# Kernel tuning notes

Measured on AMD Instinct MI355X. Metric: run time of the kernel, lower is better.

Reference implementation:

```python
import jax, jax.numpy as jnp
import numpy as np

NUM_BLOCKS = 2
NUM_LAYERS = 10
DILATIONS = tuple(2 ** d for _ in range(NUM_BLOCKS) for d in range(NUM_LAYERS))  # 20 layers
B, CIN, C, T = 8, 1, 128, 16384
L = len(DILATIONS)


def setup_inputs() -> dict:
    key = jax.random.key(0)
    ks = jax.random.split(key, 12)
    s = 0.1  # weight scale ~ kaiming-ish for C=128
    return {
        "x": jax.random.normal(ks[0], (B, CIN, T), jnp.float32),
        "W_in": jax.random.normal(ks[1], (C, CIN, 1), jnp.float32) * 0.5,
        "b_in": jnp.zeros((C,), jnp.float32),
        "W_dil": jax.random.normal(ks[2], (L, C, C, 2), jnp.float32) * s,
        "b_dil": jnp.zeros((L, C), jnp.float32),
        "W_tanh": jax.random.normal(ks[3], (L, C, C, 1), jnp.float32) * s,
        "b_tanh": jnp.zeros((L, C), jnp.float32),
        "W_sig": jax.random.normal(ks[4], (L, C, C, 1), jnp.float32) * s,
        "b_sig": jnp.zeros((L, C), jnp.float32),
        "W_skip": jax.random.normal(ks[5], (L, C, C, 1), jnp.float32) * s,
        "b_skip": jnp.zeros((L, C), jnp.float32),
    }


def _conv1x1(w, b, x):
    # w: [O, I, 1], x: [B, I, T] -> [B, O, T]
    return jnp.einsum('oi,bit->bot', w[:, :, 0], x) + b[None, :, None]


def _dilated_causal_conv(x, w, b, dilation):
    # causal pad left by (kernel_size-1)*dilation = dilation, then dilated conv k=2
    xp = jnp.pad(x, ((0, 0), (0, 0), (dilation, 0)))
    y = jax.lax.conv_general_dilated(
        xp, w, window_strides=(1,), padding=[(0, 0)],
        rhs_dilation=(dilation,), dimension_numbers=('NCW', 'OIW', 'NCW'))
    return y + b[None, :, None]


def reference(x, W_in, b_in, W_dil, b_dil, W_tanh, b_tanh, W_sig, b_sig, W_skip, b_skip):
    h = _conv1x1(W_in, b_in, x)  # [B, C, T]
    skip_agg = jnp.zeros_like(h[:, :1, :]) * 0.0  # placeholder; replaced on first add
    skip_agg = 0.0
    for l, dil in enumerate(DILATIONS):
        xd = _dilated_causal_conv(h, W_dil[l], b_dil[l], dil)
        f = jnp.tanh(_conv1x1(W_tanh[l], b_tanh[l], xd))
        g = jax.nn.sigmoid(_conv1x1(W_sig[l], b_sig[l], xd))
        xh = g * f
        skip_agg = skip_agg + _conv1x1(W_skip[l], b_skip[l], xh)
        h = xh + xd  # faithful: residual adds dilated-conv output, not layer input
    return skip_agg
```

## Files before the change

kernel.cpp:

```cpp
#include <hip/hip_runtime.h>

#define B_ 8
#define C_ 128
#define T_ 16384
#define L_ 20
#define TN 128
#define NTL (T_ / TN)
#define XROW 136
#define WROW 40

typedef short bf16x8 __attribute__((ext_vector_type(8)));
typedef float f32x16 __attribute__((ext_vector_type(16)));

__device__ __forceinline__ ushort bf16_rn(float v) {
    union { float f; unsigned u; } a; a.f = v;
    unsigned r = (a.u + 0x7FFFu + ((a.u >> 16) & 1u)) >> 16;
    return (ushort)r;
}
__device__ __forceinline__ float bf16_to_f(ushort h) {
    union { unsigned u; float f; } b; b.u = ((unsigned)h) << 16;
    return b.f;
}
__device__ __forceinline__ void split2(float v, ushort& hh, ushort& ll) {
    ushort h = bf16_rn(v);
    hh = h;
    ll = bf16_rn(v - bf16_to_f(h));
}

__global__ __launch_bounds__(256) void prep_kernel(
    const float* __restrict__ Wd, const float* __restrict__ Wt,
    const float* __restrict__ Ws, const float* __restrict__ Wk,
    ushort* __restrict__ WdH, ushort* __restrict__ WdL,
    ushort* __restrict__ WtH, ushort* __restrict__ WtL,
    ushort* __restrict__ WsH, ushort* __restrict__ WsL,
    ushort* __restrict__ WkH, ushort* __restrict__ WkL)
{
    int idx = blockIdx.x * 256 + threadIdx.x;
    const int ND = L_ * C_ * 256;
    const int N1 = L_ * C_ * C_;
    float v; ushort* oH; ushort* oL; int o;
    if (idx < ND) {
        int k = idx & 255, m = (idx >> 8) & 127, l = idx >> 15;
        v = Wd[(((size_t)(l * C_ + m)) * C_ + (k & 127)) * 2 + (k >> 7)];
        oH = WdH; oL = WdL; o = idx;
    } else {
        int i2 = idx - ND;
        if (i2 < N1)            { v = Wt[i2]; oH = WtH; oL = WtL; o = i2; }
        else if (i2 < 2 * N1)   { o = i2 - N1;     v = Ws[o]; oH = WsH; oL = WsL; }
        else if (i2 < 3 * N1)   { o = i2 - 2 * N1; v = Wk[o]; oH = WkH; oL = WkL; }
        else return;
    }
    ushort h, l; split2(v, h, l);
    oH[o] = h; oL[o] = l;
}

__global__ __launch_bounds__(256) void in_conv_kernel(
    const float* __restrict__ x, const float* __restrict__ Win,
    const float* __restrict__ bin, float* __restrict__ h)
{
    int idx = blockIdx.x * 256 + threadIdx.x;
    int t4 = idx & (T_ / 4 - 1);
    int bc = idx >> 12;
    int c = bc & 127;
    float w = Win[c], bias = bin[c];
    const float4 xv = *(const float4*)(x + ((size_t)(bc >> 7)) * T_ + (size_t)t4 * 4);
    float4 o;
    o.x = w * xv.x + bias; o.y = w * xv.y + bias;
    o.z = w * xv.z + bias; o.w = w * xv.w + bias;
    *(float4*)(h + (size_t)bc * T_ + (size_t)t4 * 4) = o;
}

__device__ __forceinline__ void stageX(
    const float* __restrict__ hb, int tbase,
    ushort* __restrict__ XH, ushort* __restrict__ XL)
{
    __syncthreads();
    const int tid = threadIdx.x;
    const int tl = tid & 127, cg = tid >> 7;
    const int tg = tbase + tl;
    const bool ok = (tg >= 0);
    #pragma unroll
    for (int j = 0; j < 8; ++j) {
        int c0 = cg * 32 + j * 4;
        float v0 = ok ? hb[(c0 + 0) * T_ + tg] : 0.f;
        float v1 = ok ? hb[(c0 + 1) * T_ + tg] : 0.f;
        float v2 = ok ? hb[(c0 + 2) * T_ + tg] : 0.f;
        float v3 = ok ? hb[(c0 + 3) * T_ + tg] : 0.f;
        ushort4 h4, l4;
        split2(v0, h4.x, l4.x); split2(v1, h4.y, l4.y);
        split2(v2, h4.z, l4.z); split2(v3, h4.w, l4.w);
        *(ushort4*)&XH[tl * XROW + c0] = h4;
        *(ushort4*)&XL[tl * XROW + c0] = l4;
    }
    __syncthreads();
}

__device__ __forceinline__ void gemm_one(
    const ushort* __restrict__ gH, const ushort* __restrict__ gL,
    int rowlen, int kw0,
    ushort* __restrict__ sH, ushort* __restrict__ sL,
    const ushort* __restrict__ XH, const ushort* __restrict__ XL,
    int m_wave, int n_wave, int ln31, int kg,
    f32x16 (&acc)[2])
{
    const int tid = threadIdx.x;
    const int sm = tid >> 2, sk = (tid & 3) * 8;
    const int gbase = sm * rowlen + kw0 + sk;
    uint4 pH = *(const uint4*)(gH + gbase);
    uint4 pL = *(const uint4*)(gL + gbase);
    #pragma unroll
    for (int c = 0; c < 4; ++c) {
        __syncthreads();
        *(uint4*)&sH[sm * WROW + sk] = pH;
        *(uint4*)&sL[sm * WROW + sk] = pL;
        int kn = (c < 3) ? (c + 1) * 32 : 3 * 32;
        pH = *(const uint4*)(gH + gbase + kn);
        pL = *(const uint4*)(gL + gbase + kn);
        __syncthreads();
        #pragma unroll
        for (int ks = 0; ks < 32; ks += 16) {
            bf16x8 bh = *(const bf16x8*)&XH[(n_wave + ln31) * XROW + c * 32 + ks + kg];
            bf16x8 bl = *(const bf16x8*)&XL[(n_wave + ln31) * XROW + c * 32 + ks + kg];
            #pragma unroll
            for (int mi = 0; mi < 2; ++mi) {
                bf16x8 ah = *(const bf16x8*)&sH[(m_wave + mi * 32 + ln31) * WROW + ks + kg];
                bf16x8 al = *(const bf16x8*)&sL[(m_wave + mi * 32 + ln31) * WROW + ks + kg];
                acc[mi] = __builtin_amdgcn_mfma_f32_32x32x16_bf16(ah, bh, acc[mi], 0, 0, 0);
                acc[mi] = __builtin_amdgcn_mfma_f32_32x32x16_bf16(ah, bl, acc[mi], 0, 0, 0);
                acc[mi] = __builtin_amdgcn_mfma_f32_32x32x16_bf16(al, bh, acc[mi], 0, 0, 0);
            }
        }
    }
}

__device__ __forceinline__ void gemm_two(
    const ushort* __restrict__ gH0, const ushort* __restrict__ gL0,
    const ushort* __restrict__ gH1, const ushort* __restrict__ gL1,
    ushort* __restrict__ sH0, ushort* __restrict__ sL0,
    ushort* __restrict__ sH1, ushort* __restrict__ sL1,
    const ushort* __restrict__ XH, const ushort* __restrict__ XL,
    int m_wave, int n_wave, int ln31, int kg,
    f32x16 (&a0)[2], f32x16 (&a1)[2])
{
    const int tid = threadIdx.x;
    const int sm = tid >> 2, sk = (tid & 3) * 8;
    const int gbase = sm * 128 + sk;
    uint4 pH0 = *(const uint4*)(gH0 + gbase);
    uint4 pL0 = *(const uint4*)(gL0 + gbase);
    uint4 pH1 = *(const uint4*)(gH1 + gbase);
    uint4 pL1 = *(const uint4*)(gL1 + gbase);
    #pragma unroll
    for (int c = 0; c < 4; ++c) {
        __syncthreads();
        *(uint4*)&sH0[sm * WROW + sk] = pH0;
        *(uint4*)&sL0[sm * WROW + sk] = pL0;
        *(uint4*)&sH1[sm * WROW + sk] = pH1;
        *(uint4*)&sL1[sm * WROW + sk] = pL1;
        int kn = (c < 3) ? (c + 1) * 32 : 3 * 32;
        pH0 = *(const uint4*)(gH0 + gbase + kn);
        pL0 = *(const uint4*)(gL0 + gbase + kn);
        pH1 = *(const uint4*)(gH1 + gbase + kn);
        pL1 = *(const uint4*)(gL1 + gbase + kn);
        __syncthreads();
        #pragma unroll
        for (int ks = 0; ks < 32; ks += 16) {
            bf16x8 bh = *(const bf16x8*)&XH[(n_wave + ln31) * XROW + c * 32 + ks + kg];
            bf16x8 bl = *(const bf16x8*)&XL[(n_wave + ln31) * XROW + c * 32 + ks + kg];
            #pragma unroll
            for (int mi = 0; mi < 2; ++mi) {
                int ai = (m_wave + mi * 32 + ln31) * WROW + ks + kg;
                bf16x8 ah0 = *(const bf16x8*)&sH0[ai];
                bf16x8 al0 = *(const bf16x8*)&sL0[ai];
                bf16x8 ah1 = *(const bf16x8*)&sH1[ai];
                bf16x8 al1 = *(const bf16x8*)&sL1[ai];
                a0[mi] = __builtin_amdgcn_mfma_f32_32x32x16_bf16(ah0, bh, a0[mi], 0, 0, 0);
                a0[mi] = __builtin_amdgcn_mfma_f32_32x32x16_bf16(ah0, bl, a0[mi], 0, 0, 0);
                a0[mi] = __builtin_amdgcn_mfma_f32_32x32x16_bf16(al0, bh, a0[mi], 0, 0, 0);
                a1[mi] = __builtin_amdgcn_mfma_f32_32x32x16_bf16(ah1, bh, a1[mi], 0, 0, 0);
                a1[mi] = __builtin_amdgcn_mfma_f32_32x32x16_bf16(ah1, bl, a1[mi], 0, 0, 0);
                a1[mi] = __builtin_amdgcn_mfma_f32_32x32x16_bf16(al1, bh, a1[mi], 0, 0, 0);
            }
        }
    }
}

__global__ __launch_bounds__(512, 2) void layer_kernel(
    const float* __restrict__ h_in, float* __restrict__ h_out,
    float* __restrict__ skip,
    const ushort* __restrict__ WdH, const ushort* __restrict__ WdL,
    const ushort* __restrict__ WtH, const ushort* __restrict__ WtL,
    const ushort* __restrict__ WsH, const ushort* __restrict__ WsL,
    const ushort* __restrict__ WkH, const ushort* __restrict__ WkL,
    const float* __restrict__ bd, const float* __restrict__ bt,
    const float* __restrict__ bs, const float* __restrict__ bk,
    int dil, int addskip)
{
    __shared__ ushort XbH[TN * XROW], XbL[TN * XROW];
    __shared__ ushort WaH[C_ * WROW], WaL[C_ * WROW];
    __shared__ ushort WbH[C_ * WROW], WbL[C_ * WROW];
    __shared__ float bias_lds[512];

    const int tid = threadIdx.x;
    const int b  = blockIdx.x / NTL;
    const int t0 = (blockIdx.x % NTL) * TN;
    const int lane = tid & 63;
    const int wave = tid >> 6;
    const int m_wave = (wave & 1) * 64;
    const int n_wave = (wave >> 1) * 32;
    const int ln31 = lane & 31, kg = (lane >> 5) * 8, hi5 = lane >> 5;
    const float* hb = h_in + (size_t)b * C_ * T_;

    {
        int sec = tid >> 7;
        const float* bp = sec == 0 ? bd : (sec == 1 ? bt : (sec == 2 ? bs : bk));
        bias_lds[tid] = bp[tid & 127];
    }

    f32x16 xdacc[2];
    #pragma unroll
    for (int mi = 0; mi < 2; ++mi)
        #pragma unroll
        for (int r = 0; r < 16; ++r) xdacc[mi][r] = 0.f;

    stageX(hb, t0 - dil, XbH, XbL);
    gemm_one(WdH, WdL, 256, 0,   WaH, WaL, XbH, XbL, m_wave, n_wave, ln31, kg, xdacc);
    stageX(hb, t0,       XbH, XbL);
    gemm_one(WdH, WdL, 256, 128, WaH, WaL, XbH, XbL, m_wave, n_wave, ln31, kg, xdacc);

    __syncthreads();
    const int nn = n_wave + ln31;
    #pragma unroll
    for (int mi = 0; mi < 2; ++mi) {
        #pragma unroll
        for (int g = 0; g < 4; ++g) {
            int mloc = m_wave + mi * 32 + g * 8 + 4 * hi5;
            const float* bb = &bias_lds[mloc];
            ushort4 h4, l4;
            float v0 = xdacc[mi][g * 4 + 0] + bb[0]; xdacc[mi][g * 4 + 0] = v0;
            float v1 = xdacc[mi][g * 4 + 1] + bb[1]; xdacc[mi][g * 4 + 1] = v1;
            float v2 = xdacc[mi][g * 4 + 2] + bb[2]; xdacc[mi][g * 4 + 2] = v2;
            float v3 = xdacc[mi][g * 4 + 3] + bb[3]; xdacc[mi][g * 4 + 3] = v3;
            split2(v0, h4.x, l4.x); split2(v1, h4.y, l4.y);
            split2(v2, h4.z, l4.z); split2(v3, h4.w, l4.w);
            *(ushort4*)&XbH[nn * XROW + mloc] = h4;
            *(ushort4*)&XbL[nn * XROW + mloc] = l4;
        }
    }

    f32x16 at[2], as_[2];
    #pragma unroll
    for (int mi = 0; mi < 2; ++mi)
        #pragma unroll
        for (int r = 0; r < 16; ++r) { at[mi][r] = 0.f; as_[mi][r] = 0.f; }
    gemm_two(WtH, WtL, WsH, WsL, WaH, WaL, WbH, WbL,
             XbH, XbL, m_wave, n_wave, ln31, kg, at, as_);

    __syncthreads();
    float* hob = h_out + (size_t)b * C_ * T_;
    f32x16 xhv[2];
    #pragma unroll
    for (int mi = 0; mi < 2; ++mi) {
        #pragma unroll
        for (int g = 0; g < 4; ++g) {
            int mloc = m_wave + mi * 32 + g * 8 + 4 * hi5;
            const float* btp = &bias_lds[128 + mloc];
            const float* bsp = &bias_lds[256 + mloc];
            ushort4 h4, l4;
            #pragma unroll
            for (int j = 0; j < 4; ++j) {
                float a = at[mi][g * 4 + j] + btp[j];
                float s = as_[mi][g * 4 + j] + bsp[j];
                float f  = 2.f / (1.f + __expf(-2.f * a)) - 1.f;
                float gg = 1.f / (1.f + __expf(-s));
                float xh = f * gg;
                xhv[mi][g * 4 + j] = xh;
                ushort hh, ll; split2(xh, hh, ll);
                ((ushort*)&h4)[j] = hh; ((ushort*)&l4)[j] = ll;
                hob[(size_t)(mloc + j) * T_ + t0 + nn] = xh + xdacc[mi][g * 4 + j];
            }
            *(ushort4*)&XbH[nn * XROW + mloc] = h4;
            *(ushort4*)&XbL[nn * XROW + mloc] = l4;
        }
    }

    f32x16 ak[2];
    #pragma unroll
    for (int mi = 0; mi < 2; ++mi)
        #pragma unroll
        for (int r = 0; r < 16; ++r) ak[mi][r] = 0.f;
    gemm_one(WkH, WkL, 128, 0, WaH, WaL, XbH, XbL, m_wave, n_wave, ln31, kg, ak);

    float* skb = skip + (size_t)b * C_ * T_;
    #pragma unroll
    for (int mi = 0; mi < 2; ++mi) {
        #pragma unroll
        for (int g = 0; g < 4; ++g) {
            int mloc = m_wave + mi * 32 + g * 8 + 4 * hi5;
            const float* bkp = &bias_lds[384 + mloc];
            #pragma unroll
            for (int j = 0; j < 4; ++j) {
                float v = ak[mi][g * 4 + j] + bkp[j];
                size_t adr = (size_t)(mloc + j) * T_ + t0 + nn;
                if (addskip) v += skb[adr];
                skb[adr] = v;
            }
        }
    }
}

extern "C" void kernel_launch(void* const* d_in, const int* in_sizes, int n_in,
                              void* d_out, int out_size, void* d_ws, size_t ws_size,
                              hipStream_t stream)
{
    const float* x   = (const float*)d_in[0];
    const float* Win = (const float*)d_in[1];
    const float* bin = (const float*)d_in[2];
    const float* Wd  = (const float*)d_in[3];
    const float* bd  = (const float*)d_in[4];
    const float* Wt  = (const float*)d_in[5];
    const float* bt  = (const float*)d_in[6];
    const float* Ws  = (const float*)d_in[7];
    const float* bs  = (const float*)d_in[8];
    const float* Wk  = (const float*)d_in[9];
    const float* bk  = (const float*)d_in[10];
    float* out = (float*)d_out;

    float* ws = (float*)d_ws;
    const size_t HN = (size_t)B_ * C_ * T_;
    float* hA = ws;
    float* hB = ws + HN;
    ushort* wb = (ushort*)(ws + 2 * HN);
    const size_t ND = (size_t)L_ * C_ * 256;
    const size_t N1 = (size_t)L_ * C_ * C_;
    ushort* WdH = wb;            ushort* WdL = WdH + ND;
    ushort* WtH = WdL + ND;      ushort* WtL = WtH + N1;
    ushort* WsH = WtL + N1;      ushort* WsL = WsH + N1;
    ushort* WkH = WsL + N1;      ushort* WkL = WkH + N1;

    const int prep_total = (int)(ND + 3 * N1);
    prep_kernel<<<(prep_total + 255) / 256, 256, 0, stream>>>(
        Wd, Wt, Ws, Wk, WdH, WdL, WtH, WtL, WsH, WsL, WkH, WkL);
    in_conv_kernel<<<(B_ * C_ * (T_ / 4)) / 256, 256, 0, stream>>>(x, Win, bin, hA);

    float* hin = hA;
    float* hout = hB;
    for (int l = 0; l < L_; ++l) {
        int dil = 1 << (l % 10);
        layer_kernel<<<B_ * NTL, 512, 0, stream>>>(
            hin, hout, out,
            WdH + (size_t)l * C_ * 256, WdL + (size_t)l * C_ * 256,
            WtH + (size_t)l * C_ * C_,  WtL + (size_t)l * C_ * C_,
            WsH + (size_t)l * C_ * C_,  WsL + (size_t)l * C_ * C_,
            WkH + (size_t)l * C_ * C_,  WkL + (size_t)l * C_ * C_,
            bd + l * C_, bt + l * C_, bs + l * C_, bk + l * C_,
            dil, l > 0 ? 1 : 0);
        float* tmp = hin; hin = hout; hout = tmp;
    }
}
```

Before: 2.778 ms.

## Shrink LDS with XOR-swizzled layouts and 16-wide K chunks for higher occupancy

Weights are pre-tiled on the host-side prep kernel into 16-wide K chunks with an XOR swizzle, and the activation tile drops its row padding in favour of an XOR swizzle, so LDS per block shrinks enough to raise launch bounds from 2 to 4 blocks per CU. The fused tanh/sigmoid GEMM is split into two sequential single-weight GEMMs, removing the second weight buffer, and the dilated-conv output is recovered from LDS instead of being held in registers. The cost is twice as many K-chunk barriers and smaller per-chunk weight loads, plus register pressure under the tighter launch bound.

```diff
diff --git a/kernel.cpp b/kernel.cpp
--- a/kernel.cpp
+++ b/kernel.cpp
@@ -6,11 +6,12 @@
 #define L_ 20
 #define TN 128
 #define NTL (T_ / TN)
-#define XROW 136
-#define WROW 40
+#define XROW 128
+#define WROW 16
 
 typedef short bf16x8 __attribute__((ext_vector_type(8)));
 typedef float f32x16 __attribute__((ext_vector_type(16)));
+typedef unsigned short u16x8 __attribute__((ext_vector_type(8)));
 
 __device__ __forceinline__ ushort bf16_rn(float v) {
     union { float f; unsigned u; } a; a.f = v;
@@ -42,16 +43,21 @@
     if (idx < ND) {
         int k = idx & 255, m = (idx >> 8) & 127, l = idx >> 15;
         v = Wd[(((size_t)(l * C_ + m)) * C_ + (k & 127)) * 2 + (k >> 7)];
-        oH = WdH; oL = WdL; o = idx;
+        o = l * (C_ * 256) + (k >> 4) * 2048 + m * WROW + ((k & 15) ^ ((m & 1) << 3));
+        oH = WdH; oL = WdL;
     } else {
         int i2 = idx - ND;
-        if (i2 < N1)            { v = Wt[i2]; oH = WtH; oL = WtL; o = i2; }
-        else if (i2 < 2 * N1)   { o = i2 - N1;     v = Ws[o]; oH = WsH; oL = WsL; }
-        else if (i2 < 3 * N1)   { o = i2 - 2 * N1; v = Wk[o]; oH = WkH; oL = WkL; }
+        const float* src;
+        if (i2 < N1)           { src = Wt; oH = WtH; oL = WtL; }
+        else if (i2 < 2 * N1)  { i2 -= N1;     src = Ws; oH = WsH; oL = WsL; }
+        else if (i2 < 3 * N1)  { i2 -= 2 * N1; src = Wk; oH = WkH; oL = WkL; }
         else return;
-    }
-    ushort h, l; split2(v, h, l);
-    oH[o] = h; oL[o] = l;
+        int k = i2 & 127, m = (i2 >> 7) & 127, l = i2 >> 14;
+        v = src[i2];
+        o = l * (C_ * C_) + (k >> 4) * 2048 + m * WROW + ((k & 15) ^ ((m & 1) << 3));
+    }
+    ushort h, l2; split2(v, h, l2);
+    oH[o] = h; oL[o] = l2;
 }
 
 __global__ __launch_bounds__(256) void in_conv_kernel(
@@ -79,112 +85,62 @@
     const int tl = tid & 127, cg = tid >> 7;
     const int tg = tbase + tl;
     const bool ok = (tg >= 0);
-    #pragma unroll
-    for (int j = 0; j < 8; ++j) {
-        int c0 = cg * 32 + j * 4;
-        float v0 = ok ? hb[(c0 + 0) * T_ + tg] : 0.f;
-        float v1 = ok ? hb[(c0 + 1) * T_ + tg] : 0.f;
-        float v2 = ok ? hb[(c0 + 2) * T_ + tg] : 0.f;
-        float v3 = ok ? hb[(c0 + 3) * T_ + tg] : 0.f;
-        ushort4 h4, l4;
-        split2(v0, h4.x, l4.x); split2(v1, h4.y, l4.y);
-        split2(v2, h4.z, l4.z); split2(v3, h4.w, l4.w);
-        *(ushort4*)&XH[tl * XROW + c0] = h4;
-        *(ushort4*)&XL[tl * XROW + c0] = l4;
+    const int sw = (tl & 7) << 3;
+    #pragma unroll
+    for (int j = 0; j < 4; ++j) {
+        int c0 = cg * 32 + j * 8;
+        u16x8 h8, l8;
+        #pragma unroll
+        for (int i = 0; i < 8; ++i) {
+            float v = ok ? hb[(size_t)(c0 + i) * T_ + tg] : 0.f;
+            ushort hh, ll; split2(v, hh, ll);
+            h8[i] = hh; l8[i] = ll;
+        }
+        *(u16x8*)&XH[tl * XROW + (c0 ^ sw)] = h8;
+        *(u16x8*)&XL[tl * XROW + (c0 ^ sw)] = l8;
     }
     __syncthreads();
 }
 
-__device__ __forceinline__ void gemm_one(
-    const ushort* __restrict__ gH, const ushort* __restrict__ gL,
-    int rowlen, int kw0,
+__device__ __forceinline__ void gemm16(
+    const ushort* __restrict__ gH, const ushort* __restrict__ gL, int kc0,
     ushort* __restrict__ sH, ushort* __restrict__ sL,
     const ushort* __restrict__ XH, const ushort* __restrict__ XL,
-    int m_wave, int n_wave, int ln31, int kg,
+    int m_wave, int nn, int ln31, int kg,
     f32x16 (&acc)[2])
 {
     const int tid = threadIdx.x;
-    const int sm = tid >> 2, sk = (tid & 3) * 8;
-    const int gbase = sm * rowlen + kw0 + sk;
-    uint4 pH = *(const uint4*)(gH + gbase);
-    uint4 pL = *(const uint4*)(gL + gbase);
-    #pragma unroll
-    for (int c = 0; c < 4; ++c) {
+    const int e = tid * 4;
+    const ushort* gph = gH + kc0 * 2048 + e;
+    const ushort* gpl = gL + kc0 * 2048 + e;
+    uint2 pH = *(const uint2*)gph;
+    uint2 pL = *(const uint2*)gpl;
+    const int nsw = (nn & 7) << 3;
+    const int a0 = (m_wave + ln31) * WROW + (kg ^ ((ln31 & 1) << 3));
+    #pragma unroll
+    for (int c = 0; c < 8; ++c) {
         __syncthreads();
-        *(uint4*)&sH[sm * WROW + sk] = pH;
-        *(uint4*)&sL[sm * WROW + sk] = pL;
-        int kn = (c < 3) ? (c + 1) * 32 : 3 * 32;
-        pH = *(const uint4*)(gH + gbase + kn);
-        pL = *(const uint4*)(gL + gbase + kn);
+        *(uint2*)&sH[e] = pH;
+        *(uint2*)&sL[e] = pL;
+        int nx = ((c < 7) ? (c + 1) : 7) * 2048;
+        pH = *(const uint2*)(gph + nx);
+        pL = *(const uint2*)(gpl + nx);
         __syncthreads();
-        #pragma unroll
-        for (int ks = 0; ks < 32; ks += 16) {
-            bf16x8 bh = *(const bf16x8*)&XH[(n_wave + ln31) * XROW + c * 32 + ks + kg];
-            bf16x8 bl = *(const bf16x8*)&XL[(n_wave + ln31) * XROW + c * 32 + ks + kg];
-            #pragma unroll
-            for (int mi = 0; mi < 2; ++mi) {
-                bf16x8 ah = *(const bf16x8*)&sH[(m_wave + mi * 32 + ln31) * WROW + ks + kg];
-                bf16x8 al = *(const bf16x8*)&sL[(m_wave + mi * 32 + ln31) * WROW + ks + kg];
-                acc[mi] = __builtin_amdgcn_mfma_f32_32x32x16_bf16(ah, bh, acc[mi], 0, 0, 0);
-                acc[mi] = __builtin_amdgcn_mfma_f32_32x32x16_bf16(ah, bl, acc[mi], 0, 0, 0);
-                acc[mi] = __builtin_amdgcn_mfma_f32_32x32x16_bf16(al, bh, acc[mi], 0, 0, 0);
-            }
-        }
-    }
-}
-
-__device__ __forceinline__ void gemm_two(
-    const ushort* __restrict__ gH0, const ushort* __restrict__ gL0,
-    const ushort* __restrict__ gH1, const ushort* __restrict__ gL1,
-    ushort* __restrict__ sH0, ushort* __restrict__ sL0,
-    ushort* __restrict__ sH1, ushort* __restrict__ sL1,
-    const ushort* __restrict__ XH, const ushort* __restrict__ XL,
-    int m_wave, int n_wave, int ln31, int kg,
-    f32x16 (&a0)[2], f32x16 (&a1)[2])
-{
-    const int tid = threadIdx.x;
-    const int sm = tid >> 2, sk = (tid & 3) * 8;
-    const int gbase = sm * 128 + sk;
-    uint4 pH0 = *(const uint4*)(gH0 + gbase);
-    uint4 pL0 = *(const uint4*)(gL0 + gbase);
-    uint4 pH1 = *(const uint4*)(gH1 + gbase);
-    uint4 pL1 = *(const uint4*)(gL1 + gbase);
-    #pragma unroll
-    for (int c = 0; c < 4; ++c) {
-        __syncthreads();
-        *(uint4*)&sH0[sm * WROW + sk] = pH0;
-        *(uint4*)&sL0[sm * WROW + sk] = pL0;
-        *(uint4*)&sH1[sm * WROW + sk] = pH1;
-        *(uint4*)&sL1[sm * WROW + sk] = pL1;
-        int kn = (c < 3) ? (c + 1) * 32 : 3 * 32;
-        pH0 = *(const uint4*)(gH0 + gbase + kn);
-        pL0 = *(const uint4*)(gL0 + gbase + kn);
-        pH1 = *(const uint4*)(gH1 + gbase + kn);
-        pL1 = *(const uint4*)(gL1 + gbase + kn);
-        __syncthreads();
-        #pragma unroll
-        for (int ks = 0; ks < 32; ks += 16) {
-            bf16x8 bh = *(const bf16x8*)&XH[(n_wave + ln31) * XROW + c * 32 + ks + kg];
-            bf16x8 bl = *(const bf16x8*)&XL[(n_wave + ln31) * XROW + c * 32 + ks + kg];
-            #pragma unroll
-            for (int mi = 0; mi < 2; ++mi) {
-                int ai = (m_wave + mi * 32 + ln31) * WROW + ks + kg;
-                bf16x8 ah0 = *(const bf16x8*)&sH0[ai];
-                bf16x8 al0 = *(const bf16x8*)&sL0[ai];
-                bf16x8 ah1 = *(const bf16x8*)&sH1[ai];
-                bf16x8 al1 = *(const bf16x8*)&sL1[ai];
-                a0[mi] = __builtin_amdgcn_mfma_f32_32x32x16_bf16(ah0, bh, a0[mi], 0, 0, 0);
-                a0[mi] = __builtin_amdgcn_mfma_f32_32x32x16_bf16(ah0, bl, a0[mi], 0, 0, 0);
-                a0[mi] = __builtin_amdgcn_mfma_f32_32x32x16_bf16(al0, bh, a0[mi], 0, 0, 0);
-                a1[mi] = __builtin_amdgcn_mfma_f32_32x32x16_bf16(ah1, bh, a1[mi], 0, 0, 0);
-                a1[mi] = __builtin_amdgcn_mfma_f32_32x32x16_bf16(ah1, bl, a1[mi], 0, 0, 0);
-                a1[mi] = __builtin_amdgcn_mfma_f32_32x32x16_bf16(al1, bh, a1[mi], 0, 0, 0);
-            }
-        }
-    }
-}
-
-__global__ __launch_bounds__(512, 2) void layer_kernel(
+        int bcol = c * 16 + kg;
+        bf16x8 bh = *(const bf16x8*)&XH[nn * XROW + (bcol ^ nsw)];
+        bf16x8 bl = *(const bf16x8*)&XL[nn * XROW + (bcol ^ nsw)];
+        #pragma unroll
+        for (int mi = 0; mi < 2; ++mi) {
+            bf16x8 ah = *(const bf16x8*)&sH[a0 + mi * 32 * WROW];
+            bf16x8 al = *(const bf16x8*)&sL[a0 + mi * 32 * WROW];
+            acc[mi] = __builtin_amdgcn_mfma_f32_32x32x16_bf16(ah, bh, acc[mi], 0, 0, 0);
+            acc[mi] = __builtin_amdgcn_mfma_f32_32x32x16_bf16(ah, bl, acc[mi], 0, 0, 0);
+            acc[mi] = __builtin_amdgcn_mfma_f32_32x32x16_bf16(al, bh, acc[mi], 0, 0, 0);
+        }
+    }
+}
+
+__global__ __launch_bounds__(512, 4) void layer_kernel(
     const float* __restrict__ h_in, float* __restrict__ h_out,
     float* __restrict__ skip,
     const ushort* __restrict__ WdH, const ushort* __restrict__ WdL,
@@ -197,7 +153,6 @@
 {
     __shared__ ushort XbH[TN * XROW], XbL[TN * XROW];
     __shared__ ushort WaH[C_ * WROW], WaL[C_ * WROW];
-    __shared__ ushort WbH[C_ * WROW], WbL[C_ * WROW];
     __shared__ float bias_lds[512];
 
     const int tid = threadIdx.x;
@@ -208,6 +163,8 @@
     const int m_wave = (wave & 1) * 64;
     const int n_wave = (wave >> 1) * 32;
     const int ln31 = lane & 31, kg = (lane >> 5) * 8, hi5 = lane >> 5;
+    const int nn = n_wave + ln31;
+    const int nsw = (nn & 7) << 3;
     const float* hb = h_in + (size_t)b * C_ * T_;
 
     {
@@ -223,63 +180,62 @@
         for (int r = 0; r < 16; ++r) xdacc[mi][r] = 0.f;
 
     stageX(hb, t0 - dil, XbH, XbL);
-    gemm_one(WdH, WdL, 256, 0,   WaH, WaL, XbH, XbL, m_wave, n_wave, ln31, kg, xdacc);
+    gemm16(WdH, WdL, 0, WaH, WaL, XbH, XbL, m_wave, nn, ln31, kg, xdacc);
     stageX(hb, t0,       XbH, XbL);
-    gemm_one(WdH, WdL, 256, 128, WaH, WaL, XbH, XbL, m_wave, n_wave, ln31, kg, xdacc);
+    gemm16(WdH, WdL, 8, WaH, WaL, XbH, XbL, m_wave, nn, ln31, kg, xdacc);
 
     __syncthreads();
-    const int nn = n_wave + ln31;
     #pragma unroll
     for (int mi = 0; mi < 2; ++mi) {
         #pragma unroll
         for (int g = 0; g < 4; ++g) {
             int mloc = m_wave + mi * 32 + g * 8 + 4 * hi5;
-            const float* bb = &bias_lds[mloc];
-            ushort4 h4, l4;
-            float v0 = xdacc[mi][g * 4 + 0] + bb[0]; xdacc[mi][g * 4 + 0] = v0;
-            float v1 = xdacc[mi][g * 4 + 1] + bb[1]; xdacc[mi][g * 4 + 1] = v1;
-            float v2 = xdacc[mi][g * 4 + 2] + bb[2]; xdacc[mi][g * 4 + 2] = v2;
-            float v3 = xdacc[mi][g * 4 + 3] + bb[3]; xdacc[mi][g * 4 + 3] = v3;
-            split2(v0, h4.x, l4.x); split2(v1, h4.y, l4.y);
-            split2(v2, h4.z, l4.z); split2(v3, h4.w, l4.w);
-            *(ushort4*)&XbH[nn * XROW + mloc] = h4;
-            *(ushort4*)&XbL[nn * XROW + mloc] = l4;
-        }
-    }
-
-    f32x16 at[2], as_[2];
-    #pragma unroll
-    for (int mi = 0; mi < 2; ++mi)
-        #pragma unroll
-        for (int r = 0; r < 16; ++r) { at[mi][r] = 0.f; as_[mi][r] = 0.f; }
-    gemm_two(WtH, WtL, WsH, WsL, WaH, WaL, WbH, WbL,
-             XbH, XbL, m_wave, n_wave, ln31, kg, at, as_);
-
-    __syncthreads();
-    float* hob = h_out + (size_t)b * C_ * T_;
-    f32x16 xhv[2];
-    #pragma unroll
-    for (int mi = 0; mi < 2; ++mi) {
-        #pragma unroll
-        for (int g = 0; g < 4; ++g) {
-            int mloc = m_wave + mi * 32 + g * 8 + 4 * hi5;
-            const float* btp = &bias_lds[128 + mloc];
-            const float* bsp = &bias_lds[256 + mloc];
             ushort4 h4, l4;
             #pragma unroll
             for (int j = 0; j < 4; ++j) {
-                float a = at[mi][g * 4 + j] + btp[j];
-                float s = as_[mi][g * 4 + j] + bsp[j];
+                float v = xdacc[mi][g * 4 + j] + bias_lds[mloc + j];
+                ushort hh, ll; split2(v, hh, ll);
+                ((ushort*)&h4)[j] = hh; ((ushort*)&l4)[j] = ll;
+            }
+            *(ushort4*)&XbH[nn * XROW + (mloc ^ nsw)] = h4;
+            *(ushort4*)&XbL[nn * XROW + (mloc ^ nsw)] = l4;
+        }
+    }
+
+    f32x16 at[2], as_[2];
+    #pragma unroll
+    for (int mi = 0; mi < 2; ++mi)
+        #pragma unroll
+        for (int r = 0; r < 16; ++r) { at[mi][r] = 0.f; as_[mi][r] = 0.f; }
+    gemm16(WtH, WtL, 0, WaH, WaL, XbH, XbL, m_wave, nn, ln31, kg, at);
+    gemm16(WsH, WsL, 0, WaH, WaL, XbH, XbL, m_wave, nn, ln31, kg, as_);
+
+    __syncthreads();
+    float* hob = h_out + (size_t)b * C_ * T_;
+    #pragma unroll
+    for (int mi = 0; mi < 2; ++mi) {
+        #pragma unroll
+        for (int g = 0; g < 4; ++g) {
+            int mloc = m_wave + mi * 32 + g * 8 + 4 * hi5;
+            int xcol = mloc ^ nsw;
+            ushort4 xdh = *(ushort4*)&XbH[nn * XROW + xcol];
+            ushort4 xdl = *(ushort4*)&XbL[nn * XROW + xcol];
+            ushort4 h4, l4;
+            #pragma unroll
+            for (int j = 0; j < 4; ++j) {
+                float a = at[mi][g * 4 + j] + bias_lds[128 + mloc + j];
+                float s = as_[mi][g * 4 + j] + bias_lds[256 + mloc + j];
                 float f  = 2.f / (1.f + __expf(-2.f * a)) - 1.f;
                 float gg = 1.f / (1.f + __expf(-s));
                 float xh = f * gg;
-                xhv[mi][g * 4 + j] = xh;
+                float xd = bf16_to_f(((const ushort*)&xdh)[j])
+                         + bf16_to_f(((const ushort*)&xdl)[j]);
+                hob[(size_t)(mloc + j) * T_ + t0 + nn] = xh + xd;
                 ushort hh, ll; split2(xh, hh, ll);
                 ((ushort*)&h4)[j] = hh; ((ushort*)&l4)[j] = ll;
-                hob[(size_t)(mloc + j) * T_ + t0 + nn] = xh + xdacc[mi][g * 4 + j];
             }
-            *(ushort4*)&XbH[nn * XROW + mloc] = h4;
-            *(ushort4*)&XbL[nn * XROW + mloc] = l4;
+            *(ushort4*)&XbH[nn * XROW + xcol] = h4;
+            *(ushort4*)&XbL[nn * XROW + xcol] = l4;
         }
     }
 
@@ -288,7 +244,7 @@
     for (int mi = 0; mi < 2; ++mi)
         #pragma unroll
         for (int r = 0; r < 16; ++r) ak[mi][r] = 0.f;
-    gemm_one(WkH, WkL, 128, 0, WaH, WaL, XbH, XbL, m_wave, n_wave, ln31, kg, ak);
+    gemm16(WkH, WkL, 0, WaH, WaL, XbH, XbL, m_wave, nn, ln31, kg, ak);
 
     float* skb = skip + (size_t)b * C_ * T_;
     #pragma unroll
@@ -296,10 +252,9 @@
         #pragma unroll
         for (int g = 0; g < 4; ++g) {
             int mloc = m_wave + mi * 32 + g * 8 + 4 * hi5;
-            const float* bkp = &bias_lds[384 + mloc];
             #pragma unroll
             for (int j = 0; j < 4; ++j) {
-                float v = ak[mi][g * 4 + j] + bkp[j];
+                float v = ak[mi][g * 4 + j] + bias_lds[384 + mloc + j];
                 size_t adr = (size_t)(mloc + j) * T_ + t0 + nn;
                 if (addskip) v += skb[adr];
                 skb[adr] = v;
```

Measured after the change: 2.360 ms. 1.18x faster.
